# Optimization experiments

Hardware: AMD Instinct MI355X
Metric: run time of the kernel (lower is better)

Reference implementation:

```python
import jax, jax.numpy as jnp
import numpy as np

DIM = 1024
NUM_HEADS = 16
NUM_KV_HEADS = 4
HEAD_DIM = DIM // NUM_HEADS
KV_DIM = NUM_KV_HEADS * HEAD_DIM
PARTIAL_ROPE_DIM = 32
ROPE_BASE = 10000.0
LORA_RANK = 4
NUM_LORA_STEPS = 2
LORA_SCALE = 1.0
B, S = 2, 2048


def _rms_norm(x):
    eps = jnp.asarray(jnp.finfo(x.dtype).eps, x.dtype)
    return x * jax.lax.rsqrt(jnp.mean(x * x, axis=-1, keepdims=True) + eps)


def _rope_cos_sin(seq_len, dtype):
    half = PARTIAL_ROPE_DIM // 2
    inv_freq = 1.0 / (ROPE_BASE ** (jnp.arange(0, PARTIAL_ROPE_DIM, 2, dtype=jnp.float32) / PARTIAL_ROPE_DIM))
    t = jnp.arange(seq_len, dtype=jnp.float32)
    freqs = jnp.outer(t, inv_freq)  # [S, half]
    return jnp.cos(freqs).astype(dtype), jnp.sin(freqs).astype(dtype)


def _apply_rope_partial(x, cos, sin):
    # x: [B, H, S, D]; rotate first PARTIAL_ROPE_DIM dims, pass the rest.
    half = PARTIAL_ROPE_DIM // 2
    x1 = x[..., :half]
    x2 = x[..., half:PARTIAL_ROPE_DIM]
    xp = x[..., PARTIAL_ROPE_DIM:]
    c = cos[None, None, :, :]
    s = sin[None, None, :, :]
    return jnp.concatenate([x1 * c + x2 * s, -x1 * s + x2 * c, xp], axis=-1)


def setup_inputs() -> dict:
    key = jax.random.key(0)
    ks = jax.random.split(key, 12)
    std = 0.02
    return {
        "x": jax.random.normal(ks[0], (B, S, DIM), jnp.float32),
        "Wq": jax.random.normal(ks[1], (DIM, DIM), jnp.float32) * std,
        "Wk": jax.random.normal(ks[2], (KV_DIM, DIM), jnp.float32) * std,
        "Wv": jax.random.normal(ks[3], (KV_DIM, DIM), jnp.float32) * std,
        "Wproj": jax.random.normal(ks[4], (DIM, DIM), jnp.float32) * std,
        "q_gain": jnp.full((NUM_HEADS,), 1.0, jnp.float32),
        "lora_A_q": jax.random.normal(ks[5], (NUM_LORA_STEPS, LORA_RANK, DIM), jnp.float32) * std,
        "lora_B_q": jax.random.normal(ks[6], (NUM_LORA_STEPS, DIM, LORA_RANK), jnp.float32) * std,
        "lora_A_v": jax.random.normal(ks[7], (NUM_LORA_STEPS, LORA_RANK, DIM), jnp.float32) * std,
        "lora_B_v": jax.random.normal(ks[8], (NUM_LORA_STEPS, KV_DIM, LORA_RANK), jnp.float32) * std,
        "step_idx": 0,
    }


def reference(x, Wq, Wk, Wv, Wproj, q_gain, lora_A_q, lora_B_q, lora_A_v, lora_B_v, step_idx):
    bsz, seqlen, dim = x.shape
    q = x @ Wq.T
    v = x @ Wv.T
    if 0 <= step_idx < NUM_LORA_STEPS:
        q = q + LORA_SCALE * ((x @ lora_A_q[step_idx].T) @ lora_B_q[step_idx].T)
        v = v + LORA_SCALE * ((x @ lora_A_v[step_idx].T) @ lora_B_v[step_idx].T)
    k = x @ Wk.T

    q = q.reshape(bsz, seqlen, NUM_HEADS, HEAD_DIM).transpose(0, 2, 1, 3)      # [B,H,S,D]
    k = k.reshape(bsz, seqlen, NUM_KV_HEADS, HEAD_DIM).transpose(0, 2, 1, 3)   # [B,Hkv,S,D]
    v = v.reshape(bsz, seqlen, NUM_KV_HEADS, HEAD_DIM).transpose(0, 2, 1, 3)

    q = _rms_norm(q)
    k = _rms_norm(k)

    cos, sin = _rope_cos_sin(seqlen, q.dtype)
    q = _apply_rope_partial(q, cos, sin)
    k = _apply_rope_partial(k, cos, sin)

    q = q * q_gain.astype(q.dtype)[None, :, None, None]

    # GQA causal SDPA
    groups = NUM_HEADS // NUM_KV_HEADS
    qg = q.reshape(bsz, NUM_KV_HEADS, groups, seqlen, HEAD_DIM)
    scale = 1.0 / np.sqrt(HEAD_DIM)
    scores = jnp.einsum('bkgsd,bktd->bkgst', qg, k) * scale  # [B,Hkv,G,S,S]
    causal = jnp.tril(jnp.ones((seqlen, seqlen), bool))
    scores = jnp.where(causal[None, None, None], scores, jnp.asarray(-jnp.inf, scores.dtype))
    attn = jax.nn.softmax(scores, axis=-1)
    y = jnp.einsum('bkgst,bktd->bkgsd', attn, v)
    y = y.reshape(bsz, NUM_HEADS, seqlen, HEAD_DIM).transpose(0, 2, 1, 3).reshape(bsz, seqlen, dim)
    return y @ Wproj.T
```

## Files before the change

### kernel.cpp

```cpp
#include <hip/hip_runtime.h>
#include <hip/hip_bf16.h>
#include <stdint.h>

#define DIM 1024
#define NH 16
#define NKV 4
#define HD 64
#define SEQ 2048
#define BATCH 2
#define RANK 4
#define NSTEPS 2

#define XN      4194304
#define WQ_END  5242880
#define WK_END  5505024
#define WV_END  5767168
#define CVT_BLOCKS 6656
#define LORA_BLOCKS 1024

typedef unsigned short u16;
typedef unsigned int u32;
typedef __attribute__((ext_vector_type(8))) __bf16 bf16x8;
typedef __attribute__((ext_vector_type(4))) float f32x4;

__device__ __forceinline__ float bf2f(u16 v) {
    u32 u = ((u32)v) << 16;
    return __builtin_bit_cast(float, u);
}
__device__ __forceinline__ u16 f2bf(float f) {
    u32 u = __builtin_bit_cast(u32, f);
    u32 r = (u + 0x7fffu + ((u >> 16) & 1u)) >> 16;
    return (u16)r;
}
__device__ __forceinline__ u32 pk2(float a, float b) {
    return (u32)f2bf(a) | ((u32)f2bf(b) << 16);
}
__device__ __forceinline__ u32 pk2t(float a, float b) {
    return __builtin_amdgcn_perm(__builtin_bit_cast(u32, b),
                                 __builtin_bit_cast(u32, a), 0x07060302u);
}
__device__ __forceinline__ void glds16(const u16* g, u16* l) {
    __builtin_amdgcn_global_load_lds(
        (const __attribute__((address_space(1))) u32*)g,
        (__attribute__((address_space(3))) u32*)l, 16, 0, 0);
}

__global__ __launch_bounds__(256) void k_prep(
    const float* __restrict__ x, const float* __restrict__ Wq,
    const float* __restrict__ Wk, const float* __restrict__ Wv,
    const float* __restrict__ Wp, u16* __restrict__ dst,
    const float* __restrict__ Aq, const float* __restrict__ Av,
    const int* __restrict__ step_p, float* __restrict__ tq, float* __restrict__ tv)
{
    int bx = blockIdx.x;
    if (bx < CVT_BLOCKS) {
        int e = (bx * 256 + threadIdx.x) * 4;
        const float* src;
        if (e < XN)          src = x  + e;
        else if (e < WQ_END) src = Wq + (e - XN);
        else if (e < WK_END) src = Wk + (e - WQ_END);
        else if (e < WV_END) src = Wv + (e - WK_END);
        else                 src = Wp + (e - WV_END);
        float4 v = *(const float4*)src;
        *(uint2*)(dst + e) = make_uint2(pk2(v.x, v.y), pk2(v.z, v.w));
        return;
    }
    int wave = ((bx - CVT_BLOCKS) * 256 + threadIdx.x) >> 6;
    int lane = threadIdx.x & 63;
    int step = step_p[0];
    int valid = (step >= 0 && step < NSTEPS);
    int sc = valid ? step : 0;
    const float* xr = x + wave * DIM + lane * 16;
    float xf[16];
#pragma unroll
    for (int q = 0; q < 4; q++) {
        float4 v4 = *(const float4*)(xr + q * 4);
        xf[q * 4 + 0] = v4.x; xf[q * 4 + 1] = v4.y;
        xf[q * 4 + 2] = v4.z; xf[q * 4 + 3] = v4.w;
    }
    float sums[8];
#pragma unroll
    for (int j = 0; j < 8; j++) {
        const float* ar = (j < 4 ? Aq + sc * RANK * DIM + j * DIM
                                 : Av + sc * RANK * DIM + (j - 4) * DIM) + lane * 16;
        float s = 0.f;
#pragma unroll
        for (int q = 0; q < 4; q++) {
            float4 a4 = *(const float4*)(ar + q * 4);
            s += xf[q * 4 + 0] * a4.x + xf[q * 4 + 1] * a4.y
               + xf[q * 4 + 2] * a4.z + xf[q * 4 + 3] * a4.w;
        }
#pragma unroll
        for (int o = 32; o > 0; o >>= 1) s += __shfl_xor(s, o, 64);
        sums[j] = s;
    }
    if (!valid) {
#pragma unroll
        for (int j = 0; j < 8; j++) sums[j] = 0.f;
    }
    if (lane == 0) {
        tq[wave * 4 + 0] = sums[0]; tq[wave * 4 + 1] = sums[1];
        tq[wave * 4 + 2] = sums[2]; tq[wave * 4 + 3] = sums[3];
        tv[wave * 4 + 0] = sums[4]; tv[wave * 4 + 1] = sums[5];
        tv[wave * 4 + 2] = sums[6]; tv[wave * 4 + 3] = sums[7];
    }
}

__global__ __launch_bounds__(256) void k_gemm_qkv(
    const u16* __restrict__ A, const u16* __restrict__ B,
    u16* __restrict__ qkv, u16* __restrict__ vtb,
    const float* __restrict__ tq, const float* __restrict__ Bq,
    const float* __restrict__ tv, const float* __restrict__ Bv,
    const float* __restrict__ gain, const int* __restrict__ step_p)
{
    __shared__ __align__(16) u16 As[8192];
    __shared__ __align__(16) u16 Bs[8192];
    int bx = blockIdx.x;
    int xcd = bx & 7, o = bx >> 3;
    int bm = xcd * 4 + (o & 3);
    int bn = o >> 2;
    int t = threadIdx.x, lane = t & 63, w = t >> 6;
    int wy = w >> 1, wx = w & 1;
    int wb = t & ~63;
    int quad = lane >> 4, n16 = lane & 15;
    f32x4 acc[4][4];
#pragma unroll
    for (int i = 0; i < 4; i++)
#pragma unroll
        for (int j = 0; j < 4; j++) acc[i][j] = (f32x4){0.f, 0.f, 0.f, 0.f};

    int goff[4];
#pragma unroll
    for (int u = 0; u < 4; u++) {
        int idx = u * 256 + t;
        int grp = idx >> 6;
        int q_ = (idx >> 4) & 3, m = idx & 15;
        goff[u] = ((grp >> 1) * 16 + m) * DIM + (grp & 1) * 32 + q_ * 8;
    }
    const u16* Ab = A + bm * 128 * DIM;
    const u16* Bb = B + bn * 128 * DIM;

#pragma unroll 1
    for (int kb = 0; kb < 16; kb++) {
        int k0 = kb * 64;
        __syncthreads();
#pragma unroll
        for (int u = 0; u < 4; u++)
            glds16(Ab + goff[u] + k0, As + (u * 256 + wb) * 8);
#pragma unroll
        for (int u = 0; u < 4; u++)
            glds16(Bb + goff[u] + k0, Bs + (u * 256 + wb) * 8);
        __syncthreads();
#pragma unroll
        for (int c = 0; c < 2; c++) {
            bf16x8 af[4], bfr[4];
#pragma unroll
            for (int i = 0; i < 4; i++)
                af[i] = *(const bf16x8*)(As + (((wy * 4 + i) * 2 + c) * 64 + lane) * 8);
#pragma unroll
            for (int j = 0; j < 4; j++)
                bfr[j] = *(const bf16x8*)(Bs + (((wx * 4 + j) * 2 + c) * 64 + lane) * 8);
#pragma unroll
            for (int i = 0; i < 4; i++)
#pragma unroll
                for (int j = 0; j < 4; j++)
                    acc[i][j] = __builtin_amdgcn_mfma_f32_16x16x32_bf16(af[i], bfr[j], acc[i][j], 0, 0, 0);
        }
    }

    int step = step_p[0];
    int sc = (step >= 0 && step < NSTEPS) ? step : 0;
    int row_base = bm * 128 + wy * 64 + quad * 4;

    if (bn < 10) {
        bool isq = (bn < 8);
        int h2 = isq ? (bn * 2 + wx) : ((bn - 8) * 2 + wx);
        int colbase = isq ? (h2 * 64) : (1024 + h2 * 64);
        if (isq) {
            float4 B4[4];
#pragma unroll
            for (int j = 0; j < 4; j++)
                B4[j] = *(const float4*)(Bq + (sc * DIM + h2 * 64 + j * 16 + n16) * RANK);
#pragma unroll
            for (int i = 0; i < 4; i++)
#pragma unroll
                for (int r = 0; r < 4; r++) {
                    float4 t4 = *(const float4*)(tq + (row_base + i * 16 + r) * 4);
#pragma unroll
                    for (int j = 0; j < 4; j++)
                        acc[i][j][r] += t4.x * B4[j].x + t4.y * B4[j].y
                                      + t4.z * B4[j].z + t4.w * B4[j].w;
                }
        }
        float postmul = isq ? (gain[h2] * 0.125f * 1.4426950408889634f) : 1.f;
        float invf = exp2f(-(float)n16 * 0.8304820237218405f);
#pragma unroll
        for (int i = 0; i < 4; i++)
#pragma unroll
            for (int r = 0; r < 4; r++) {
                float s = acc[i][0][r] * acc[i][0][r] + acc[i][1][r] * acc[i][1][r]
                        + acc[i][2][r] * acc[i][2][r] + acc[i][3][r] * acc[i][3][r];
#pragma unroll
                for (int o2 = 1; o2 < 16; o2 <<= 1) s += __shfl_xor(s, o2, 64);
                float rr = rsqrtf(s * (1.f / 64.f) + 1.1920928955078125e-7f);
                int row = row_base + i * 16 + r;
                float v0 = acc[i][0][r] * rr, v1 = acc[i][1][r] * rr;
                float v2 = acc[i][2][r] * rr, v3 = acc[i][3][r] * rr;
                float ang = (float)(row & 2047) * invf;
                float cs = cosf(ang), sn = sinf(ang);
                float o0 = v0 * cs + v1 * sn;
                float o1 = -v0 * sn + v1 * cs;
                u16* dst = qkv + row * 1536 + colbase + n16;
                dst[0]  = f2bf(o0 * postmul);
                dst[16] = f2bf(o1 * postmul);
                dst[32] = f2bf(v2 * postmul);
                dst[48] = f2bf(v3 * postmul);
            }
    } else {
        int g = (bn - 10) * 2 + wx;
        float4 B4[4];
#pragma unroll
        for (int j = 0; j < 4; j++)
            B4[j] = *(const float4*)(Bv + (sc * (NKV * HD) + g * 64 + j * 16 + n16) * RANK);
#pragma unroll
        for (int i = 0; i < 4; i++) {
#pragma unroll
            for (int r = 0; r < 4; r++) {
                float4 t4 = *(const float4*)(tv + (row_base + i * 16 + r) * 4);
#pragma unroll
                for (int j = 0; j < 4; j++)
                    acc[i][j][r] += t4.x * B4[j].x + t4.y * B4[j].y
                                  + t4.z * B4[j].z + t4.w * B4[j].w;
            }
            int row0 = row_base + i * 16;
            int b = row0 >> 11, s0 = row0 & 2047;
#pragma unroll
            for (int j = 0; j < 4; j++) {
                int d = j * 16 + n16;
                uint2 pkv = make_uint2(pk2(acc[i][j][0], acc[i][j][1]),
                                       pk2(acc[i][j][2], acc[i][j][3]));
                *(uint2*)(vtb + ((b * NKV + g) * HD + d) * SEQ + s0) = pkv;
            }
        }
    }
}

__global__ __launch_bounds__(256) void k_gemm_proj(
    const u16* __restrict__ A, const u16* __restrict__ B,
    float* __restrict__ C)
{
    __shared__ __align__(16) u16 As[8192];
    __shared__ __align__(16) u16 Bs[4096];
    int bx = blockIdx.x;
    int bn = (bx & 7) * 2 + ((bx >> 3) & 1);
    int bm = bx >> 4;
    int t = threadIdx.x, lane = t & 63, w = t >> 6;
    int wy = w >> 1, wx = w & 1;
    int wb = t & ~63;
    f32x4 acc[4][2];
#pragma unroll
    for (int i = 0; i < 4; i++)
#pragma unroll
        for (int j = 0; j < 2; j++) acc[i][j] = (f32x4){0.f, 0.f, 0.f, 0.f};

    int goffA[4], goffB[2];
#pragma unroll
    for (int u = 0; u < 4; u++) {
        int idx = u * 256 + t;
        int grp = idx >> 6;
        int q_ = (idx >> 4) & 3, m = idx & 15;
        goffA[u] = ((grp >> 1) * 16 + m) * DIM + (grp & 1) * 32 + q_ * 8;
    }
#pragma unroll
    for (int u = 0; u < 2; u++) {
        int idx = u * 256 + t;
        int grp = idx >> 6;
        int q_ = (idx >> 4) & 3, m = idx & 15;
        goffB[u] = ((grp >> 1) * 16 + m) * DIM + (grp & 1) * 32 + q_ * 8;
    }
    const u16* Ab = A + bm * 128 * DIM;
    const u16* Bb = B + bn * 64 * DIM;

#pragma unroll 1
    for (int kb = 0; kb < 16; kb++) {
        int k0 = kb * 64;
        __syncthreads();
#pragma unroll
        for (int u = 0; u < 4; u++)
            glds16(Ab + goffA[u] + k0, As + (u * 256 + wb) * 8);
#pragma unroll
        for (int u = 0; u < 2; u++)
            glds16(Bb + goffB[u] + k0, Bs + (u * 256 + wb) * 8);
        __syncthreads();
#pragma unroll
        for (int c = 0; c < 2; c++) {
            bf16x8 af[4], bfr[2];
#pragma unroll
            for (int i = 0; i < 4; i++)
                af[i] = *(const bf16x8*)(As + (((wy * 4 + i) * 2 + c) * 64 + lane) * 8);
#pragma unroll
            for (int j = 0; j < 2; j++)
                bfr[j] = *(const bf16x8*)(Bs + (((wx * 2 + j) * 2 + c) * 64 + lane) * 8);
#pragma unroll
            for (int i = 0; i < 4; i++)
#pragma unroll
                for (int j = 0; j < 2; j++)
                    acc[i][j] = __builtin_amdgcn_mfma_f32_16x16x32_bf16(af[i], bfr[j], acc[i][j], 0, 0, 0);
        }
    }
    int quad = lane >> 4, n16 = lane & 15;
#pragma unroll
    for (int i = 0; i < 4; i++)
#pragma unroll
        for (int j = 0; j < 2; j++) {
            int col = bn * 64 + wx * 32 + j * 16 + n16;
#pragma unroll
            for (int r = 0; r < 4; r++) {
                int rowm = bm * 128 + wy * 64 + i * 16 + quad * 4 + r;
                C[rowm * DIM + col] = acc[i][j][r];
            }
        }
}

__global__ __launch_bounds__(256) void k_attn(
    const u16* __restrict__ qkv, const u16* __restrict__ vt,
    const float* __restrict__ gain, u16* __restrict__ y)
{
    __shared__ __align__(16) u16 kf[2][4096];
    __shared__ __align__(16) u16 vf[2][4096];
    __shared__ __align__(16) u16 pb[4][1024];
    int bx = blockIdx.x;
    int bgid = bx & 7, inner = bx >> 3;
    int b = bgid >> 2, g = bgid & 3;
    int h = g * 4 + (inner & 3);
    int qtsel = (inner >> 2) & 15;
    int t = threadIdx.x, lane = t & 63, w = t >> 6, wb = t & ~63;
    int quad = lane >> 4, n16 = lane & 15;
    float negM = -11.67f * fabsf(gain[h]);

    const u16* kbase = qkv + b * SEQ * 1536 + 1024 + g * HD;
    const u16* vbase = vt + (b * NKV + g) * HD * SEQ;

    int koff0, koff1, voff0, voff1;
    {
        int s0 = t, r0 = s0 >> 3, c0 = (s0 & 7) ^ (r0 & 7);
        koff0 = r0 * 1536 + c0 * 8;  voff0 = r0 * 2048 + c0 * 8;
        int s1 = 256 + t, r1 = s1 >> 3, c1 = (s1 & 7) ^ (r1 & 7);
        koff1 = r1 * 1536 + c1 * 8;  voff1 = r1 * 2048 + c1 * 8;
    }
    int swb = n16 & 7;
    int o0 = n16 * 8 + (quad ^ swb);
    int o1 = n16 * 8 + ((4 + quad) ^ swb);
    u16* pw = pb[w];

    f32x4 accA[4], accB[4];
    float psA = 0.f, psB = 0.f;
#pragma unroll
    for (int i = 0; i < 4; i++) {
        accA[i] = (f32x4){0.f, 0.f, 0.f, 0.f};
        accB[i] = (f32x4){0.f, 0.f, 0.f, 0.f};
    }
    int qrowA = qtsel * 64 + w * 16 + n16;
    int qrowB = (31 - qtsel) * 64 + w * 16 + n16;
    bf16x8 qloA, qhiA, qloB, qhiB;
    {
        const u16* qpA = qkv + (b * SEQ + qrowA) * 1536 + h * HD + quad * 8;
        qloA = *(const bf16x8*)qpA;
        qhiA = *(const bf16x8*)(qpA + 32);
        const u16* qpB = qkv + (b * SEQ + qrowB) * 1536 + h * HD + quad * 8;
        qloB = *(const bf16x8*)qpB;
        qhiB = *(const bf16x8*)(qpB + 32);
    }

    auto stage = [&](int kt, int p) {
        const u16* kp = kbase + kt * (64 * 1536);
        const u16* vp = vbase + kt * 64;
        glds16(kp + koff0, kf[p] + wb * 8);
        glds16(kp + koff1, kf[p] + (256 + wb) * 8);
        glds16(vp + voff0, vf[p] + wb * 8);
        glds16(vp + voff1, vf[p] + (256 + wb) * 8);
    };
    auto tilecomp = [&](f32x4* acc, float& ps, bf16x8 qlo, bf16x8 qhi,
                        int qrow, int kt, int p, bool diag) {
        f32x4 st[4];
        __builtin_amdgcn_s_setprio(1);
#pragma unroll
        for (int nt = 0; nt < 4; nt++) {
            f32x4 sa = (f32x4){0.f, 0.f, 0.f, 0.f};
            sa = __builtin_amdgcn_mfma_f32_16x16x32_bf16(*(bf16x8*)(kf[p] + (nt * 128 + o0) * 8), qlo, sa, 0, 0, 0);
            sa = __builtin_amdgcn_mfma_f32_16x16x32_bf16(*(bf16x8*)(kf[p] + (nt * 128 + o1) * 8), qhi, sa, 0, 0, 0);
            st[nt] = sa;
        }
        __builtin_amdgcn_s_setprio(0);
        float pr[4][4];
        if (diag) {
            int kb0 = kt * 64;
#pragma unroll
            for (int nt = 0; nt < 4; nt++)
#pragma unroll
                for (int r = 0; r < 4; r++) {
                    int key = kb0 + nt * 16 + quad * 4 + r;
                    float e = exp2f(st[nt][r] + negM);
                    e = (key > qrow) ? 0.f : e;
                    pr[nt][r] = e;
                    ps += e;
                }
        } else {
#pragma unroll
            for (int nt = 0; nt < 4; nt++)
#pragma unroll
                for (int r = 0; r < 4; r++) {
                    float e = exp2f(st[nt][r] + negM);
                    pr[nt][r] = e;
                    ps += e;
                }
        }
#pragma unroll
        for (int nt = 0; nt < 4; nt++) {
            u32 lo = pk2t(pr[nt][0], pr[nt][1]);
            u32 hi = pk2t(pr[nt][2], pr[nt][3]);
            int ck = nt >> 1;
            int qbk = (nt & 1) * 2 + (quad >> 1);
            int byteoff = (ck * 64 + qbk * 16 + n16) * 16 + (quad & 1) * 8;
            *(uint2*)((char*)pw + byteoff) = make_uint2(lo, hi);
        }
        asm volatile("s_waitcnt lgkmcnt(0)" ::: "memory");
        __builtin_amdgcn_s_setprio(1);
#pragma unroll
        for (int ck = 0; ck < 2; ck++) {
            bf16x8 pfr = *(bf16x8*)(pw + (ck * 64 + lane) * 8);
            int oo = ck ? o1 : o0;
#pragma unroll
            for (int dt = 0; dt < 4; dt++)
                acc[dt] = __builtin_amdgcn_mfma_f32_16x16x32_bf16(*(bf16x8*)(vf[p] + (dt * 128 + oo) * 8), pfr, acc[dt], 0, 0, 0);
        }
        __builtin_amdgcn_s_setprio(0);
        asm volatile("" ::: "memory");
    };
    auto finish = [&](f32x4* acc, float ps, int qrow) {
        float pt = ps + __shfl_xor(ps, 16, 64);
        pt += __shfl_xor(pt, 32, 64);
        float li = 1.f / pt;
#pragma unroll
        for (int dt = 0; dt < 4; dt++) {
            uint2 o = make_uint2(pk2(acc[dt][0] * li, acc[dt][1] * li),
                                 pk2(acc[dt][2] * li, acc[dt][3] * li));
            int d = dt * 16 + quad * 4;
            *(uint2*)(y + (b * SEQ + qrow) * DIM + h * HD + d) = o;
        }
    };

    int ktEnd = 32 - qtsel;
    int p = 0;
    stage(0, 0);
#pragma unroll 1
    for (int kt = 0; kt < ktEnd; kt++) {
        if (kt + 1 < ktEnd) {
            stage(kt + 1, p ^ 1);
            asm volatile("s_waitcnt vmcnt(4)" ::: "memory");
        } else {
            asm volatile("s_waitcnt vmcnt(0)" ::: "memory");
        }
        __builtin_amdgcn_s_barrier();
        if (kt <= qtsel)
            tilecomp(accA, psA, qloA, qhiA, qrowA, kt, p, kt == qtsel);
        tilecomp(accB, psB, qloB, qhiB, qrowB, kt, p, kt == ktEnd - 1);
        asm volatile("s_waitcnt lgkmcnt(0)" ::: "memory");
        __builtin_amdgcn_s_barrier();
        p ^= 1;
    }
    finish(accA, psA, qrowA);
    finish(accB, psB, qrowB);
}

extern "C" void kernel_launch(void* const* d_in, const int* in_sizes, int n_in,
                              void* d_out, int out_size, void* d_ws, size_t ws_size,
                              hipStream_t stream)
{
    (void)in_sizes; (void)n_in; (void)out_size; (void)ws_size;
    const float* x     = (const float*)d_in[0];
    const float* Wq    = (const float*)d_in[1];
    const float* Wk    = (const float*)d_in[2];
    const float* Wv    = (const float*)d_in[3];
    const float* Wproj = (const float*)d_in[4];
    const float* qgain = (const float*)d_in[5];
    const float* Aq    = (const float*)d_in[6];
    const float* Bq    = (const float*)d_in[7];
    const float* Av    = (const float*)d_in[8];
    const float* Bv    = (const float*)d_in[9];
    const int*   step  = (const int*)d_in[10];

    char* ws = (char*)d_ws;
    u16* wsbf = (u16*)ws;
    u16* xb   = wsbf;
    u16* wf   = wsbf + XN;
    u16* wp   = wsbf + WV_END;
    u16* qkv  = (u16*)(ws + 13631488);
    float* tq = (float*)(ws + 26214400);
    float* tv = tq + 16384;
    u16* vt   = (u16*)(ws + 26607616);
    u16* y    = xb;

    k_prep<<<CVT_BLOCKS + LORA_BLOCKS, 256, 0, stream>>>(x, Wq, Wk, Wv, Wproj, wsbf,
                                                         Aq, Av, step, tq, tv);
    k_gemm_qkv<<<384, 256, 0, stream>>>(xb, wf, qkv, vt, tq, Bq, tv, Bv, qgain, step);
    k_attn<<<512, 256, 0, stream>>>(qkv, vt, qgain, y);
    k_gemm_proj<<<512, 256, 0, stream>>>(y, wp, (float*)d_out);
}
```

Measured before the change: 209.1 us.

## Replace paired causal query tiles with one tile per block, longest first

```diff
diff --git a/kernel.cpp b/kernel.cpp
--- a/kernel.cpp
+++ b/kernel.cpp
@@ -333,7 +333,7 @@
     int bgid = bx & 7, inner = bx >> 3;
     int b = bgid >> 2, g = bgid & 3;
     int h = g * 4 + (inner & 3);
-    int qtsel = (inner >> 2) & 15;
+    int qt = 31 - (inner >> 2);
     int t = threadIdx.x, lane = t & 63, w = t >> 6, wb = t & ~63;
     int quad = lane >> 4, n16 = lane & 15;
     float negM = -11.67f * fabsf(gain[h]);
@@ -353,23 +353,16 @@
     int o1 = n16 * 8 + ((4 + quad) ^ swb);
     u16* pw = pb[w];
 
-    f32x4 accA[4], accB[4];
-    float psA = 0.f, psB = 0.f;
-#pragma unroll
-    for (int i = 0; i < 4; i++) {
-        accA[i] = (f32x4){0.f, 0.f, 0.f, 0.f};
-        accB[i] = (f32x4){0.f, 0.f, 0.f, 0.f};
-    }
-    int qrowA = qtsel * 64 + w * 16 + n16;
-    int qrowB = (31 - qtsel) * 64 + w * 16 + n16;
-    bf16x8 qloA, qhiA, qloB, qhiB;
+    f32x4 acc[4];
+    float ps = 0.f;
+#pragma unroll
+    for (int i = 0; i < 4; i++) acc[i] = (f32x4){0.f, 0.f, 0.f, 0.f};
+    int qrow = qt * 64 + w * 16 + n16;
+    bf16x8 qlo, qhi;
     {
-        const u16* qpA = qkv + (b * SEQ + qrowA) * 1536 + h * HD + quad * 8;
-        qloA = *(const bf16x8*)qpA;
-        qhiA = *(const bf16x8*)(qpA + 32);
-        const u16* qpB = qkv + (b * SEQ + qrowB) * 1536 + h * HD + quad * 8;
-        qloB = *(const bf16x8*)qpB;
-        qhiB = *(const bf16x8*)(qpB + 32);
+        const u16* qp = qkv + (b * SEQ + qrow) * 1536 + h * HD + quad * 8;
+        qlo = *(const bf16x8*)qp;
+        qhi = *(const bf16x8*)(qp + 32);
     }
 
     auto stage = [&](int kt, int p) {
@@ -380,8 +373,7 @@
         glds16(vp + voff0, vf[p] + wb * 8);
         glds16(vp + voff1, vf[p] + (256 + wb) * 8);
     };
-    auto tilecomp = [&](f32x4* acc, float& ps, bf16x8 qlo, bf16x8 qhi,
-                        int qrow, int kt, int p, bool diag) {
+    auto tilecomp = [&](int kt, int p, bool diag) {
         f32x4 st[4];
         __builtin_amdgcn_s_setprio(1);
 #pragma unroll
@@ -437,20 +429,8 @@
         __builtin_amdgcn_s_setprio(0);
         asm volatile("" ::: "memory");
     };
-    auto finish = [&](f32x4* acc, float ps, int qrow) {
-        float pt = ps + __shfl_xor(ps, 16, 64);
-        pt += __shfl_xor(pt, 32, 64);
-        float li = 1.f / pt;
-#pragma unroll
-        for (int dt = 0; dt < 4; dt++) {
-            uint2 o = make_uint2(pk2(acc[dt][0] * li, acc[dt][1] * li),
-                                 pk2(acc[dt][2] * li, acc[dt][3] * li));
-            int d = dt * 16 + quad * 4;
-            *(uint2*)(y + (b * SEQ + qrow) * DIM + h * HD + d) = o;
-        }
-    };
-
-    int ktEnd = 32 - qtsel;
+
+    int ktEnd = qt + 1;
     int p = 0;
     stage(0, 0);
 #pragma unroll 1
@@ -462,15 +442,23 @@
             asm volatile("s_waitcnt vmcnt(0)" ::: "memory");
         }
         __builtin_amdgcn_s_barrier();
-        if (kt <= qtsel)
-            tilecomp(accA, psA, qloA, qhiA, qrowA, kt, p, kt == qtsel);
-        tilecomp(accB, psB, qloB, qhiB, qrowB, kt, p, kt == ktEnd - 1);
+        tilecomp(kt, p, kt == ktEnd - 1);
         asm volatile("s_waitcnt lgkmcnt(0)" ::: "memory");
         __builtin_amdgcn_s_barrier();
         p ^= 1;
     }
-    finish(accA, psA, qrowA);
-    finish(accB, psB, qrowB);
+    {
+        float pt = ps + __shfl_xor(ps, 16, 64);
+        pt += __shfl_xor(pt, 32, 64);
+        float li = 1.f / pt;
+#pragma unroll
+        for (int dt = 0; dt < 4; dt++) {
+            uint2 o = make_uint2(pk2(acc[dt][0] * li, acc[dt][1] * li),
+                                 pk2(acc[dt][2] * li, acc[dt][3] * li));
+            int d = dt * 16 + quad * 4;
+            *(uint2*)(y + (b * SEQ + qrow) * DIM + h * HD + d) = o;
+        }
+    }
 }
 
 extern "C" void kernel_launch(void* const* d_in, const int* in_sizes, int n_in,
@@ -504,6 +492,6 @@
     k_prep<<<CVT_BLOCKS + LORA_BLOCKS, 256, 0, stream>>>(x, Wq, Wk, Wv, Wproj, wsbf,
                                                          Aq, Av, step, tq, tv);
     k_gemm_qkv<<<384, 256, 0, stream>>>(xb, wf, qkv, vt, tq, Bq, tv, Bv, qgain, step);
-    k_attn<<<512, 256, 0, stream>>>(qkv, vt, qgain, y);
+    k_attn<<<1024, 256, 0, stream>>>(qkv, vt, qgain, y);
     k_gemm_proj<<<512, 256, 0, stream>>>(y, wp, (float*)d_out);
 }
```

Result: no change. 207.1 us (median of 3 runs) (-1.0%).

## Interleave both query tiles in attention loop to share K/V LDS fragment loads

Applied to the files above, without the earlier changes.

```diff
diff --git a/kernel.cpp b/kernel.cpp
--- a/kernel.cpp
+++ b/kernel.cpp
@@ -328,7 +328,7 @@
 {
     __shared__ __align__(16) u16 kf[2][4096];
     __shared__ __align__(16) u16 vf[2][4096];
-    __shared__ __align__(16) u16 pb[4][1024];
+    __shared__ __align__(16) u16 pb[4][2][1024];
     int bx = blockIdx.x;
     int bgid = bx & 7, inner = bx >> 3;
     int b = bgid >> 2, g = bgid & 3;
@@ -351,7 +351,8 @@
     int swb = n16 & 7;
     int o0 = n16 * 8 + (quad ^ swb);
     int o1 = n16 * 8 + ((4 + quad) ^ swb);
-    u16* pw = pb[w];
+    u16* pwA = pb[w][0];
+    u16* pwB = pb[w][1];
 
     f32x4 accA[4], accB[4];
     float psA = 0.f, psB = 0.f;
@@ -380,75 +381,6 @@
         glds16(vp + voff0, vf[p] + wb * 8);
         glds16(vp + voff1, vf[p] + (256 + wb) * 8);
     };
-    auto tilecomp = [&](f32x4* acc, float& ps, bf16x8 qlo, bf16x8 qhi,
-                        int qrow, int kt, int p, bool diag) {
-        f32x4 st[4];
-        __builtin_amdgcn_s_setprio(1);
-#pragma unroll
-        for (int nt = 0; nt < 4; nt++) {
-            f32x4 sa = (f32x4){0.f, 0.f, 0.f, 0.f};
-            sa = __builtin_amdgcn_mfma_f32_16x16x32_bf16(*(bf16x8*)(kf[p] + (nt * 128 + o0) * 8), qlo, sa, 0, 0, 0);
-            sa = __builtin_amdgcn_mfma_f32_16x16x32_bf16(*(bf16x8*)(kf[p] + (nt * 128 + o1) * 8), qhi, sa, 0, 0, 0);
-            st[nt] = sa;
-        }
-        __builtin_amdgcn_s_setprio(0);
-        float pr[4][4];
-        if (diag) {
-            int kb0 = kt * 64;
-#pragma unroll
-            for (int nt = 0; nt < 4; nt++)
-#pragma unroll
-                for (int r = 0; r < 4; r++) {
-                    int key = kb0 + nt * 16 + quad * 4 + r;
-                    float e = exp2f(st[nt][r] + negM);
-                    e = (key > qrow) ? 0.f : e;
-                    pr[nt][r] = e;
-                    ps += e;
-                }
-        } else {
-#pragma unroll
-            for (int nt = 0; nt < 4; nt++)
-#pragma unroll
-                for (int r = 0; r < 4; r++) {
-                    float e = exp2f(st[nt][r] + negM);
-                    pr[nt][r] = e;
-                    ps += e;
-                }
-        }
-#pragma unroll
-        for (int nt = 0; nt < 4; nt++) {
-            u32 lo = pk2t(pr[nt][0], pr[nt][1]);
-            u32 hi = pk2t(pr[nt][2], pr[nt][3]);
-            int ck = nt >> 1;
-            int qbk = (nt & 1) * 2 + (quad >> 1);
-            int byteoff = (ck * 64 + qbk * 16 + n16) * 16 + (quad & 1) * 8;
-            *(uint2*)((char*)pw + byteoff) = make_uint2(lo, hi);
-        }
-        asm volatile("s_waitcnt lgkmcnt(0)" ::: "memory");
-        __builtin_amdgcn_s_setprio(1);
-#pragma unroll
-        for (int ck = 0; ck < 2; ck++) {
-            bf16x8 pfr = *(bf16x8*)(pw + (ck * 64 + lane) * 8);
-            int oo = ck ? o1 : o0;
-#pragma unroll
-            for (int dt = 0; dt < 4; dt++)
-                acc[dt] = __builtin_amdgcn_mfma_f32_16x16x32_bf16(*(bf16x8*)(vf[p] + (dt * 128 + oo) * 8), pfr, acc[dt], 0, 0, 0);
-        }
-        __builtin_amdgcn_s_setprio(0);
-        asm volatile("" ::: "memory");
-    };
-    auto finish = [&](f32x4* acc, float ps, int qrow) {
-        float pt = ps + __shfl_xor(ps, 16, 64);
-        pt += __shfl_xor(pt, 32, 64);
-        float li = 1.f / pt;
-#pragma unroll
-        for (int dt = 0; dt < 4; dt++) {
-            uint2 o = make_uint2(pk2(acc[dt][0] * li, acc[dt][1] * li),
-                                 pk2(acc[dt][2] * li, acc[dt][3] * li));
-            int d = dt * 16 + quad * 4;
-            *(uint2*)(y + (b * SEQ + qrow) * DIM + h * HD + d) = o;
-        }
-    };
 
     int ktEnd = 32 - qtsel;
     int p = 0;
@@ -462,15 +394,174 @@
             asm volatile("s_waitcnt vmcnt(0)" ::: "memory");
         }
         __builtin_amdgcn_s_barrier();
-        if (kt <= qtsel)
-            tilecomp(accA, psA, qloA, qhiA, qrowA, kt, p, kt == qtsel);
-        tilecomp(accB, psB, qloB, qhiB, qrowB, kt, p, kt == ktEnd - 1);
+        bool actA = (kt <= qtsel);
+        bool diagA = (kt == qtsel);
+        bool diagB = (kt == ktEnd - 1);
+
+        f32x4 stA[4], stB[4];
+        __builtin_amdgcn_s_setprio(1);
+        {
+            bf16x8 kh[4];
+#pragma unroll
+            for (int nt = 0; nt < 4; nt++)
+                kh[nt] = *(bf16x8*)(kf[p] + (nt * 128 + o0) * 8);
+#pragma unroll
+            for (int nt = 0; nt < 4; nt++) {
+                f32x4 z = (f32x4){0.f, 0.f, 0.f, 0.f};
+                stB[nt] = __builtin_amdgcn_mfma_f32_16x16x32_bf16(kh[nt], qloB, z, 0, 0, 0);
+            }
+            if (actA) {
+#pragma unroll
+                for (int nt = 0; nt < 4; nt++) {
+                    f32x4 z = (f32x4){0.f, 0.f, 0.f, 0.f};
+                    stA[nt] = __builtin_amdgcn_mfma_f32_16x16x32_bf16(kh[nt], qloA, z, 0, 0, 0);
+                }
+            }
+#pragma unroll
+            for (int nt = 0; nt < 4; nt++)
+                kh[nt] = *(bf16x8*)(kf[p] + (nt * 128 + o1) * 8);
+#pragma unroll
+            for (int nt = 0; nt < 4; nt++)
+                stB[nt] = __builtin_amdgcn_mfma_f32_16x16x32_bf16(kh[nt], qhiB, stB[nt], 0, 0, 0);
+            if (actA) {
+#pragma unroll
+                for (int nt = 0; nt < 4; nt++)
+                    stA[nt] = __builtin_amdgcn_mfma_f32_16x16x32_bf16(kh[nt], qhiA, stA[nt], 0, 0, 0);
+            }
+        }
+        __builtin_amdgcn_s_setprio(0);
+
+        {
+            float pr[4][4];
+            if (diagB) {
+                int kb0 = kt * 64;
+#pragma unroll
+                for (int nt = 0; nt < 4; nt++)
+#pragma unroll
+                    for (int r = 0; r < 4; r++) {
+                        int key = kb0 + nt * 16 + quad * 4 + r;
+                        float e = exp2f(stB[nt][r] + negM);
+                        e = (key > qrowB) ? 0.f : e;
+                        pr[nt][r] = e;
+                        psB += e;
+                    }
+            } else {
+#pragma unroll
+                for (int nt = 0; nt < 4; nt++)
+#pragma unroll
+                    for (int r = 0; r < 4; r++) {
+                        float e = exp2f(stB[nt][r] + negM);
+                        pr[nt][r] = e;
+                        psB += e;
+                    }
+            }
+#pragma unroll
+            for (int nt = 0; nt < 4; nt++) {
+                u32 lo = pk2t(pr[nt][0], pr[nt][1]);
+                u32 hi = pk2t(pr[nt][2], pr[nt][3]);
+                int ck = nt >> 1;
+                int qbk = (nt & 1) * 2 + (quad >> 1);
+                int byteoff = (ck * 64 + qbk * 16 + n16) * 16 + (quad & 1) * 8;
+                *(uint2*)((char*)pwB + byteoff) = make_uint2(lo, hi);
+            }
+        }
+        if (actA) {
+            float pr[4][4];
+            if (diagA) {
+                int kb0 = kt * 64;
+#pragma unroll
+                for (int nt = 0; nt < 4; nt++)
+#pragma unroll
+                    for (int r = 0; r < 4; r++) {
+                        int key = kb0 + nt * 16 + quad * 4 + r;
+                        float e = exp2f(stA[nt][r] + negM);
+                        e = (key > qrowA) ? 0.f : e;
+                        pr[nt][r] = e;
+                        psA += e;
+                    }
+            } else {
+#pragma unroll
+                for (int nt = 0; nt < 4; nt++)
+#pragma unroll
+                    for (int r = 0; r < 4; r++) {
+                        float e = exp2f(stA[nt][r] + negM);
+                        pr[nt][r] = e;
+                        psA += e;
+                    }
+            }
+#pragma unroll
+            for (int nt = 0; nt < 4; nt++) {
+                u32 lo = pk2t(pr[nt][0], pr[nt][1]);
+                u32 hi = pk2t(pr[nt][2], pr[nt][3]);
+                int ck = nt >> 1;
+                int qbk = (nt & 1) * 2 + (quad >> 1);
+                int byteoff = (ck * 64 + qbk * 16 + n16) * 16 + (quad & 1) * 8;
+                *(uint2*)((char*)pwA + byteoff) = make_uint2(lo, hi);
+            }
+        }
+        asm volatile("s_waitcnt lgkmcnt(0)" ::: "memory");
+
+        __builtin_amdgcn_s_setprio(1);
+        {
+            bf16x8 vh[4];
+            bf16x8 pfrB = *(bf16x8*)(pwB + lane * 8);
+            bf16x8 pfrA;
+            if (actA) pfrA = *(bf16x8*)(pwA + lane * 8);
+#pragma unroll
+            for (int dt = 0; dt < 4; dt++)
+                vh[dt] = *(bf16x8*)(vf[p] + (dt * 128 + o0) * 8);
+#pragma unroll
+            for (int dt = 0; dt < 4; dt++)
+                accB[dt] = __builtin_amdgcn_mfma_f32_16x16x32_bf16(vh[dt], pfrB, accB[dt], 0, 0, 0);
+            if (actA) {
+#pragma unroll
+                for (int dt = 0; dt < 4; dt++)
+                    accA[dt] = __builtin_amdgcn_mfma_f32_16x16x32_bf16(vh[dt], pfrA, accA[dt], 0, 0, 0);
+            }
+            pfrB = *(bf16x8*)(pwB + (64 + lane) * 8);
+            if (actA) pfrA = *(bf16x8*)(pwA + (64 + lane) * 8);
+#pragma unroll
+            for (int dt = 0; dt < 4; dt++)
+                vh[dt] = *(bf16x8*)(vf[p] + (dt * 128 + o1) * 8);
+#pragma unroll
+            for (int dt = 0; dt < 4; dt++)
+                accB[dt] = __builtin_amdgcn_mfma_f32_16x16x32_bf16(vh[dt], pfrB, accB[dt], 0, 0, 0);
+            if (actA) {
+#pragma unroll
+                for (int dt = 0; dt < 4; dt++)
+                    accA[dt] = __builtin_amdgcn_mfma_f32_16x16x32_bf16(vh[dt], pfrA, accA[dt], 0, 0, 0);
+            }
+        }
+        __builtin_amdgcn_s_setprio(0);
+        asm volatile("" ::: "memory");
         asm volatile("s_waitcnt lgkmcnt(0)" ::: "memory");
         __builtin_amdgcn_s_barrier();
         p ^= 1;
     }
-    finish(accA, psA, qrowA);
-    finish(accB, psB, qrowB);
+    {
+        float pt = psA + __shfl_xor(psA, 16, 64);
+        pt += __shfl_xor(pt, 32, 64);
+        float li = 1.f / pt;
+#pragma unroll
+        for (int dt = 0; dt < 4; dt++) {
+            uint2 o = make_uint2(pk2(accA[dt][0] * li, accA[dt][1] * li),
+                                 pk2(accA[dt][2] * li, accA[dt][3] * li));
+            int d = dt * 16 + quad * 4;
+            *(uint2*)(y + (b * SEQ + qrowA) * DIM + h * HD + d) = o;
+        }
+    }
+    {
+        float pt = psB + __shfl_xor(psB, 16, 64);
+        pt += __shfl_xor(pt, 32, 64);
+        float li = 1.f / pt;
+#pragma unroll
+        for (int dt = 0; dt < 4; dt++) {
+            uint2 o = make_uint2(pk2(accB[dt][0] * li, accB[dt][1] * li),
+                                 pk2(accB[dt][2] * li, accB[dt][3] * li));
+            int d = dt * 16 + quad * 4;
+            *(uint2*)(y + (b * SEQ + qrowB) * DIM + h * HD + d) = o;
+        }
+    }
 }
 
 extern "C" void kernel_launch(void* const* d_in, const int* in_sizes, int n_in,
```

Result: slower. 216.3 us (+3.4%).
